# Kernel optimization log

Hardware: AMD Instinct MI355X
Metric: run time of the kernel (lower is better)

## Reference

```python
import jax, jax.numpy as jnp
import numpy as np

DIM = 2048
HIDDEN = 4096
BATCH = 4
SEQ = 2048


def setup_inputs() -> dict:
    key = jax.random.key(0)
    ks = jax.random.split(key, 4)
    scale_in = 1.0 / np.sqrt(DIM)
    scale_out = 1.0 / np.sqrt(HIDDEN)
    return {
        "x": jax.random.normal(ks[0], (BATCH, SEQ, DIM), dtype=jnp.float32),
        "W_in": jax.random.normal(ks[1], (HIDDEN, DIM), dtype=jnp.float32) * scale_in,
        "b_in": jnp.zeros((HIDDEN,), dtype=jnp.float32),
        "W_out": jax.random.normal(ks[2], (DIM, HIDDEN), dtype=jnp.float32) * scale_out,
        "b_out": jnp.zeros((DIM,), dtype=jnp.float32),
        "gamma": jnp.ones((HIDDEN,), dtype=jnp.float32),
        "beta": jnp.zeros((HIDDEN,), dtype=jnp.float32),
    }


def reference(x, W_in, b_in, W_out, b_out, gamma, beta):
    # Pre-project all timesteps in one GEMM: u[b,s,h] = input_proj(x[b,s,:])
    u = jnp.einsum("bsd,hd->bsh", x, W_in) + b_in  # [B,S,H]

    # Sequential elementwise recurrence: state = tanh(u_t + state*gamma + beta)
    def step(state, u_t):
        s = jnp.tanh(u_t + state * gamma + beta)
        return s, s

    init = jnp.zeros((x.shape[0], W_in.shape[0]), dtype=x.dtype)  # [B,H]
    _, states = jax.lax.scan(step, init, jnp.swapaxes(u, 0, 1))  # [S,B,H]
    states = jnp.swapaxes(states, 0, 1)  # [B,S,H]

    # Output projection in one GEMM (matches per-step out_proj then stack)
    y = jnp.einsum("bsh,dh->bsd", states, W_out) + b_out  # [B,S,D]
    return y
```

## Files before the change

### kernel.cpp

```cpp
#include <hip/hip_runtime.h>
#include <hip/hip_bf16.h>
#include <math.h>

#define B_ 4
#define S_ 2048
#define D_ 2048
#define H_ 4096
#define M_ (B_*S_)

#define SEG 128
#define WARM 48
#define P_ (S_/SEG)

typedef __bf16 bf16x8 __attribute__((ext_vector_type(8)));
typedef float f32x4 __attribute__((ext_vector_type(4)));

__device__ __forceinline__ float bf2f(unsigned short v) {
    union { unsigned u; float f; } x; x.u = ((unsigned)v) << 16; return x.f;
}
__device__ __forceinline__ unsigned short f2bf(float f) {
    union { float f; unsigned u; } x; x.f = f;
    unsigned u = x.u;
    unsigned r = (u + 0x7fffu + ((u >> 16) & 1u)) >> 16;
    return (unsigned short)r;
}

__device__ __forceinline__ float fast_exp2(float x) {
#if __has_builtin(__builtin_amdgcn_exp2f)
    return __builtin_amdgcn_exp2f(x);
#else
    return __builtin_exp2f(x);
#endif
}
__device__ __forceinline__ float fast_rcp(float x) {
    return __builtin_amdgcn_rcpf(x);
}

__global__ void cvt_f32_bf16(const float* __restrict__ in,
                             unsigned short* __restrict__ out, int n) {
    int i = (blockIdx.x * blockDim.x + threadIdx.x) * 8;
    if (i >= n) return;
    float4 a = *(const float4*)(in + i);
    float4 b = *(const float4*)(in + i + 4);
    ushort4 o0; o0.x = f2bf(a.x); o0.y = f2bf(a.y); o0.z = f2bf(a.z); o0.w = f2bf(a.w);
    ushort4 o1; o1.x = f2bf(b.x); o1.y = f2bf(b.y); o1.z = f2bf(b.z); o1.w = f2bf(b.w);
    *(ushort4*)(out + i) = o0;
    *(ushort4*)(out + i + 4) = o1;
}

__device__ __forceinline__ void async_cp16(const unsigned short* g, unsigned short* l) {
    __builtin_amdgcn_global_load_lds(
        (__attribute__((address_space(1))) void*)g,
        (__attribute__((address_space(3))) void*)l,
        16, 0, 0);
}

__device__ __forceinline__
void stage_tile(const unsigned short* Ag0, const unsigned short* Ag1,
                const unsigned short* Bg0, const unsigned short* Bg1,
                int kt, unsigned short* As, unsigned short* Bs,
                int c0, int c1) {
    async_cp16(Ag0 + kt, As + c0 * 8);
    async_cp16(Ag1 + kt, As + c1 * 8);
    async_cp16(Bg0 + kt, Bs + c0 * 8);
    async_cp16(Bg1 + kt, Bs + c1 * 8);
}

__device__ __forceinline__
void compute_tile(const unsigned short* As, const unsigned short* Bs,
                  int wr, int wc, int laneM, int laneK, f32x4 acc[4][4]) {
    bf16x8 af[4], bfr[4];
    #pragma unroll
    for (int i = 0; i < 4; ++i) {
        af[i]  = *(const bf16x8*)(As + (wr + i * 16 + laneM) * 32 + laneK);
        bfr[i] = *(const bf16x8*)(Bs + (wc + i * 16 + laneM) * 32 + laneK);
    }
    #pragma unroll
    for (int i = 0; i < 4; ++i)
        #pragma unroll
        for (int j = 0; j < 4; ++j)
            acc[i][j] = __builtin_amdgcn_mfma_f32_16x16x32_bf16(
                af[i], bfr[j], acc[i][j], 0, 0, 0);
}

template<bool OUT_BF16>
__device__ __forceinline__
void gemm_bt_body(const unsigned short* __restrict__ A,
                  const unsigned short* __restrict__ Bw,
                  const float* __restrict__ bias,
                  unsigned short* __restrict__ outB,
                  float* __restrict__ outF,
                  int M, int N, int K)
{
    __shared__ __align__(16) unsigned short As[2][128 * 32];
    __shared__ __align__(16) unsigned short Bs[2][128 * 32];

    const int tid  = threadIdx.x;
    const int lane = tid & 63;
    const int wave = tid >> 6;
    const int wr = (wave >> 1) * 64;
    const int wc = (wave & 1) * 64;

    const int row0 = blockIdx.y * 128;
    const int col0 = blockIdx.x * 128;

    const int c0 = tid, c1 = tid + 256;
    const int r0 = c0 >> 2, s0 = (c0 & 3) * 8;
    const int r1 = c1 >> 2, s1 = (c1 & 3) * 8;

    const unsigned short* Ag0 = A  + (size_t)(row0 + r0) * K + s0;
    const unsigned short* Ag1 = A  + (size_t)(row0 + r1) * K + s1;
    const unsigned short* Bg0 = Bw + (size_t)(col0 + r0) * K + s0;
    const unsigned short* Bg1 = Bw + (size_t)(col0 + r1) * K + s1;

    const int laneM = lane & 15;
    const int laneK = (lane >> 4) * 8;

    f32x4 acc[4][4];
    #pragma unroll
    for (int i = 0; i < 4; ++i)
        #pragma unroll
        for (int j = 0; j < 4; ++j)
            acc[i][j] = (f32x4){0.f, 0.f, 0.f, 0.f};

    stage_tile(Ag0, Ag1, Bg0, Bg1, 0, As[0], Bs[0], c0, c1);
    __syncthreads();

    for (int kt = 0; kt < K; kt += 64) {
        stage_tile(Ag0, Ag1, Bg0, Bg1, kt + 32, As[1], Bs[1], c0, c1);
        compute_tile(As[0], Bs[0], wr, wc, laneM, laneK, acc);
        __syncthreads();

        if (kt + 64 < K)
            stage_tile(Ag0, Ag1, Bg0, Bg1, kt + 64, As[0], Bs[0], c0, c1);
        compute_tile(As[1], Bs[1], wr, wc, laneM, laneK, acc);
        __syncthreads();
    }

    const int rQuad = (lane >> 4) * 4;
    #pragma unroll
    for (int j = 0; j < 4; ++j) {
        const int n = col0 + wc + j * 16 + laneM;
        const float bv = bias[n];
        #pragma unroll
        for (int i = 0; i < 4; ++i) {
            #pragma unroll
            for (int rr = 0; rr < 4; ++rr) {
                const int m = row0 + wr + i * 16 + rQuad + rr;
                const float v = acc[i][j][rr] + bv;
                if (OUT_BF16) outB[(size_t)m * N + n] = f2bf(v);
                else          outF[(size_t)m * N + n] = v;
            }
        }
    }
}

__global__ __launch_bounds__(256, 4)
void gemm_u(const unsigned short* __restrict__ A, const unsigned short* __restrict__ Bw,
            const float* __restrict__ bias, unsigned short* __restrict__ outB,
            int M, int N, int K) {
    gemm_bt_body<true>(A, Bw, bias, outB, nullptr, M, N, K);
}
__global__ __launch_bounds__(256, 4)
void gemm_y(const unsigned short* __restrict__ A, const unsigned short* __restrict__ Bw,
            const float* __restrict__ bias, float* __restrict__ outF,
            int M, int N, int K) {
    gemm_bt_body<false>(A, Bw, bias, nullptr, outF, M, N, K);
}

__global__ __launch_bounds__(256)
void recur_seg(const unsigned short* __restrict__ u,
               const float* __restrict__ gamma,
               const float* __restrict__ beta,
               unsigned short* __restrict__ st)
{
    const int tid = blockIdx.x * 256 + threadIdx.x;
    const int h   = tid & (H_ - 1);
    const int b   = (tid >> 12) & (B_ - 1);
    const int seg = tid >> 14;
    const int s0  = seg * SEG;
    const int sw  = (seg == 0) ? 0 : s0 - WARM;
    const int nst = s0 + SEG - sw;
    const float K2  = 2.885390082f;
    const float gk  = gamma[h] * K2;
    const float bek = beta[h]  * K2;
    float state = 0.f;

    size_t idx = ((size_t)b * S_ + sw) * H_ + h;
    float cur[16], nxt[16];
    #pragma unroll
    for (int k = 0; k < 16; ++k) cur[k] = bf2f(u[idx + (size_t)k * H_]);

    int s = sw;
    const int ngroups = nst >> 4;
    for (int g = 0; g < ngroups; ++g) {
        const size_t nidx = idx + (size_t)16 * H_;
        if (g + 1 < ngroups) {
            #pragma unroll
            for (int k = 0; k < 16; ++k) nxt[k] = bf2f(u[nidx + (size_t)k * H_]);
        }
        #pragma unroll
        for (int k = 0; k < 16; ++k) {
            const float c = fmaf(cur[k], K2, bek);
            const float t = fmaf(state, gk, c);
            const float e = fast_exp2(t);
            const float rr = fast_rcp(1.0f + e);
            state = fmaf(-2.0f, rr, 1.0f);
            if (s + k >= s0) st[idx + (size_t)k * H_] = f2bf(state);
        }
        idx = nidx; s += 16;
        #pragma unroll
        for (int k = 0; k < 16; ++k) cur[k] = nxt[k];
    }
}

extern "C" void kernel_launch(void* const* d_in, const int* in_sizes, int n_in,
                              void* d_out, int out_size, void* d_ws, size_t ws_size,
                              hipStream_t stream) {
    const float* x     = (const float*)d_in[0];
    const float* W_in  = (const float*)d_in[1];
    const float* b_in  = (const float*)d_in[2];
    const float* W_out = (const float*)d_in[3];
    const float* b_out = (const float*)d_in[4];
    const float* gamma = (const float*)d_in[5];
    const float* beta  = (const float*)d_in[6];
    float* y = (float*)d_out;

    unsigned short* x_b    = (unsigned short*)d_ws;
    unsigned short* win_b  = x_b    + (size_t)M_ * D_;
    unsigned short* wout_b = win_b  + (size_t)H_ * D_;
    unsigned short* u_b    = wout_b + (size_t)D_ * H_;
    unsigned short* st_b   = u_b    + (size_t)M_ * H_;

    cvt_f32_bf16<<<(M_ * D_) / 2048, 256, 0, stream>>>(x,     x_b,    M_ * D_);
    cvt_f32_bf16<<<(H_ * D_) / 2048, 256, 0, stream>>>(W_in,  win_b,  H_ * D_);
    cvt_f32_bf16<<<(D_ * H_) / 2048, 256, 0, stream>>>(W_out, wout_b, D_ * H_);

    dim3 g1(H_ / 128, M_ / 128);
    gemm_u<<<g1, 256, 0, stream>>>(x_b, win_b, b_in, u_b, M_, H_, D_);

    recur_seg<<<(P_ * B_ * H_) / 256, 256, 0, stream>>>(u_b, gamma, beta, st_b);

    dim3 g2(D_ / 128, M_ / 128);
    gemm_y<<<g2, 256, 0, stream>>>(st_b, wout_b, b_out, y, M_, D_, H_);
}
```

Before: 507.2 us.

## Rewrite GEMMs with 256x256 tiles, 8 waves, swizzled LDS and deeper async pipeline

Replaces the 128x128, 4-wave bf16 GEMM with a 256x256 block tile using 512 threads. Each wave computes a 128x64 sub-tile. Global-to-LDS async loads are split into half-tile stages issued several steps ahead with explicit vmcnt waits and raw barriers. An XOR swizzle on LDS offsets avoids bank conflicts, and s_setprio raises priority around the MFMA bursts. The aim is more data reuse per loaded byte and better overlap of loads with matrix math, at the cost of more registers, fewer blocks for the smaller output GEMM, and fragile hand-tuned wait counts.

```diff
diff --git a/kernel.cpp b/kernel.cpp
--- a/kernel.cpp
+++ b/kernel.cpp
@@ -55,98 +55,169 @@
         16, 0, 0);
 }
 
+__device__ __forceinline__ void fence_bar() {
+    asm volatile("" ::: "memory");
+    __builtin_amdgcn_s_barrier();
+    asm volatile("" ::: "memory");
+}
+
+template<int N>
+__device__ __forceinline__ void wait_vmcnt() {
+    if constexpr (N == 0)      asm volatile("s_waitcnt vmcnt(0)" ::: "memory");
+    else if constexpr (N == 4) asm volatile("s_waitcnt vmcnt(4)" ::: "memory");
+    else if constexpr (N == 6) asm volatile("s_waitcnt vmcnt(6)" ::: "memory");
+}
+
+
 __device__ __forceinline__
-void stage_tile(const unsigned short* Ag0, const unsigned short* Ag1,
-                const unsigned short* Bg0, const unsigned short* Bg1,
-                int kt, unsigned short* As, unsigned short* Bs,
-                int c0, int c1) {
-    async_cp16(Ag0 + kt, As + c0 * 8);
-    async_cp16(Ag1 + kt, As + c1 * 8);
-    async_cp16(Bg0 + kt, Bs + c0 * 8);
-    async_cp16(Bg1 + kt, Bs + c1 * 8);
+void stage_half(int g, int G, unsigned short (&lds)[2][2][2][8192],
+                const unsigned short* Asrc, const unsigned short* Bsrc,
+                int K, int sdst)
+{
+    if (g >= G) return;
+    const int tau = g >> 2;
+    const int mat = g & 1;
+    const int kh  = (g >> 1) & 1;
+    const unsigned short* src = (mat ? Bsrc : Asrc) + (size_t)tau * 64 + kh * 32;
+    unsigned short* dst = &lds[tau & 1][mat][kh][sdst];
+    async_cp16(src, dst);
+    async_cp16(src + (size_t)128 * K, dst + 4096);
 }
 
 __device__ __forceinline__
-void compute_tile(const unsigned short* As, const unsigned short* Bs,
-                  int wr, int wc, int laneM, int laneK, f32x4 acc[4][4]) {
-    bf16x8 af[4], bfr[4];
-    #pragma unroll
-    for (int i = 0; i < 4; ++i) {
-        af[i]  = *(const bf16x8*)(As + (wr + i * 16 + laneM) * 32 + laneK);
-        bfr[i] = *(const bf16x8*)(Bs + (wc + i * 16 + laneM) * 32 + laneK);
-    }
-    #pragma unroll
-    for (int i = 0; i < 4; ++i)
-        #pragma unroll
+void mfma16(const bf16x8* a, const bf16x8* b, f32x4 (*acc)[4]) {
+#pragma unroll
+    for (int i = 0; i < 4; ++i)
+#pragma unroll
         for (int j = 0; j < 4; ++j)
             acc[i][j] = __builtin_amdgcn_mfma_f32_16x16x32_bf16(
-                af[i], bfr[j], acc[i][j], 0, 0, 0);
+                a[i], b[j], acc[i][j], 0, 0, 0);
+}
+
+template<int BUF, int VP1, int VP3>
+__device__ __forceinline__
+void do_tile(int t, int G, unsigned short (&lds)[2][2][2][8192],
+             const unsigned short* Asrc, const unsigned short* Bsrc, int K,
+             int sdst, int aoff, int boff, f32x4 (*acc)[4])
+{
+    const int g0 = 4 * t + 5;
+    bf16x8 a[4], b[4];
+
+#pragma unroll
+    for (int j = 0; j < 4; ++j)
+        b[j] = *(const bf16x8*)(&lds[BUF][1][0][boff + j * 512]);
+#pragma unroll
+    for (int i = 0; i < 4; ++i)
+        a[i] = *(const bf16x8*)(&lds[BUF][0][0][aoff + i * 512]);
+    stage_half(g0 + 0, G, lds, Asrc, Bsrc, K, sdst);
+    fence_bar();
+    __builtin_amdgcn_s_setprio(1);
+    mfma16(a, b, acc);
+    __builtin_amdgcn_s_setprio(0);
+    fence_bar();
+
+#pragma unroll
+    for (int i = 0; i < 4; ++i)
+        a[i] = *(const bf16x8*)(&lds[BUF][0][0][aoff + (i + 4) * 512]);
+    stage_half(g0 + 1, G, lds, Asrc, Bsrc, K, sdst);
+    wait_vmcnt<VP1>();
+    fence_bar();
+    __builtin_amdgcn_s_setprio(1);
+    mfma16(a, b, acc + 4);
+    __builtin_amdgcn_s_setprio(0);
+    fence_bar();
+
+#pragma unroll
+    for (int j = 0; j < 4; ++j)
+        b[j] = *(const bf16x8*)(&lds[BUF][1][1][boff + j * 512]);
+#pragma unroll
+    for (int i = 0; i < 4; ++i)
+        a[i] = *(const bf16x8*)(&lds[BUF][0][1][aoff + i * 512]);
+    stage_half(g0 + 2, G, lds, Asrc, Bsrc, K, sdst);
+    fence_bar();
+    __builtin_amdgcn_s_setprio(1);
+    mfma16(a, b, acc);
+    __builtin_amdgcn_s_setprio(0);
+    fence_bar();
+
+#pragma unroll
+    for (int i = 0; i < 4; ++i)
+        a[i] = *(const bf16x8*)(&lds[BUF][0][1][aoff + (i + 4) * 512]);
+    stage_half(g0 + 3, G, lds, Asrc, Bsrc, K, sdst);
+    if constexpr (VP3 >= 0) wait_vmcnt<VP3>();
+    fence_bar();
+    __builtin_amdgcn_s_setprio(1);
+    mfma16(a, b, acc + 4);
+    __builtin_amdgcn_s_setprio(0);
+    fence_bar();
 }
 
 template<bool OUT_BF16>
 __device__ __forceinline__
-void gemm_bt_body(const unsigned short* __restrict__ A,
+void gemm256_body(const unsigned short* __restrict__ A,
                   const unsigned short* __restrict__ Bw,
                   const float* __restrict__ bias,
                   unsigned short* __restrict__ outB,
                   float* __restrict__ outF,
                   int M, int N, int K)
 {
-    __shared__ __align__(16) unsigned short As[2][128 * 32];
-    __shared__ __align__(16) unsigned short Bs[2][128 * 32];
+    __shared__ __align__(16) unsigned short lds[2][2][2][8192];
 
     const int tid  = threadIdx.x;
     const int lane = tid & 63;
     const int wave = tid >> 6;
-    const int wr = (wave >> 1) * 64;
-    const int wc = (wave & 1) * 64;
-
-    const int row0 = blockIdx.y * 128;
-    const int col0 = blockIdx.x * 128;
-
-    const int c0 = tid, c1 = tid + 256;
-    const int r0 = c0 >> 2, s0 = (c0 & 3) * 8;
-    const int r1 = c1 >> 2, s1 = (c1 & 3) * 8;
-
-    const unsigned short* Ag0 = A  + (size_t)(row0 + r0) * K + s0;
-    const unsigned short* Ag1 = A  + (size_t)(row0 + r1) * K + s1;
-    const unsigned short* Bg0 = Bw + (size_t)(col0 + r0) * K + s0;
-    const unsigned short* Bg1 = Bw + (size_t)(col0 + r1) * K + s1;
+    const int wm = wave >> 2;
+    const int wn = wave & 3;
+    const int row0 = blockIdx.y * 256;
+    const int col0 = blockIdx.x * 256;
+    const int NT = K >> 6;
+    const int G  = NT << 2;
+
+    const int srow = tid >> 2;
+    const int scol = ((tid & 3) ^ ((tid >> 3) & 3)) * 8;
+    const unsigned short* Asrc = A  + (size_t)(row0 + srow) * K + scol;
+    const unsigned short* Bsrc = Bw + (size_t)(col0 + srow) * K + scol;
+    const int sdst = tid * 8;
 
     const int laneM = lane & 15;
     const int laneK = (lane >> 4) * 8;
-
-    f32x4 acc[4][4];
-    #pragma unroll
-    for (int i = 0; i < 4; ++i)
-        #pragma unroll
+    const int swz   = ((laneM >> 1) & 3) << 3;
+    const int aoff  = (((wm * 128 + laneM) * 32 + laneK)) ^ swz;
+    const int boff  = (((wn * 64  + laneM) * 32 + laneK)) ^ swz;
+
+    f32x4 acc[8][4];
+#pragma unroll
+    for (int i = 0; i < 8; ++i)
+#pragma unroll
         for (int j = 0; j < 4; ++j)
             acc[i][j] = (f32x4){0.f, 0.f, 0.f, 0.f};
 
-    stage_tile(Ag0, Ag1, Bg0, Bg1, 0, As[0], Bs[0], c0, c1);
-    __syncthreads();
-
-    for (int kt = 0; kt < K; kt += 64) {
-        stage_tile(Ag0, Ag1, Bg0, Bg1, kt + 32, As[1], Bs[1], c0, c1);
-        compute_tile(As[0], Bs[0], wr, wc, laneM, laneK, acc);
-        __syncthreads();
-
-        if (kt + 64 < K)
-            stage_tile(Ag0, Ag1, Bg0, Bg1, kt + 64, As[0], Bs[0], c0, c1);
-        compute_tile(As[1], Bs[1], wr, wc, laneM, laneK, acc);
-        __syncthreads();
+    stage_half(0, G, lds, Asrc, Bsrc, K, sdst);
+    stage_half(1, G, lds, Asrc, Bsrc, K, sdst);
+    stage_half(2, G, lds, Asrc, Bsrc, K, sdst);
+    stage_half(3, G, lds, Asrc, Bsrc, K, sdst);
+    stage_half(4, G, lds, Asrc, Bsrc, K, sdst);
+    wait_vmcnt<6>();
+    fence_bar();
+
+    int t = 0;
+    for (; t < NT - 2; t += 2) {
+        do_tile<0, 6, 6>(t,     G, lds, Asrc, Bsrc, K, sdst, aoff, boff, acc);
+        do_tile<1, 6, 6>(t + 1, G, lds, Asrc, Bsrc, K, sdst, aoff, boff, acc);
     }
-
-    const int rQuad = (lane >> 4) * 4;
-    #pragma unroll
+    do_tile<0, 6, 4>(NT - 2, G, lds, Asrc, Bsrc, K, sdst, aoff, boff, acc);
+    do_tile<1, 0, -1>(NT - 1, G, lds, Asrc, Bsrc, K, sdst, aoff, boff, acc);
+
+    const int rQ = (lane >> 4) * 4;
+#pragma unroll
     for (int j = 0; j < 4; ++j) {
-        const int n = col0 + wc + j * 16 + laneM;
+        const int n = col0 + wn * 64 + j * 16 + laneM;
         const float bv = bias[n];
-        #pragma unroll
-        for (int i = 0; i < 4; ++i) {
-            #pragma unroll
+#pragma unroll
+        for (int i = 0; i < 8; ++i) {
+#pragma unroll
             for (int rr = 0; rr < 4; ++rr) {
-                const int m = row0 + wr + i * 16 + rQuad + rr;
+                const int m = row0 + wm * 128 + i * 16 + rQ + rr;
                 const float v = acc[i][j][rr] + bv;
                 if (OUT_BF16) outB[(size_t)m * N + n] = f2bf(v);
                 else          outF[(size_t)m * N + n] = v;
@@ -155,17 +226,17 @@
     }
 }
 
-__global__ __launch_bounds__(256, 4)
+__global__ __launch_bounds__(512, 2)
 void gemm_u(const unsigned short* __restrict__ A, const unsigned short* __restrict__ Bw,
             const float* __restrict__ bias, unsigned short* __restrict__ outB,
             int M, int N, int K) {
-    gemm_bt_body<true>(A, Bw, bias, outB, nullptr, M, N, K);
-}
-__global__ __launch_bounds__(256, 4)
+    gemm256_body<true>(A, Bw, bias, outB, nullptr, M, N, K);
+}
+__global__ __launch_bounds__(512, 2)
 void gemm_y(const unsigned short* __restrict__ A, const unsigned short* __restrict__ Bw,
             const float* __restrict__ bias, float* __restrict__ outF,
             int M, int N, int K) {
-    gemm_bt_body<false>(A, Bw, bias, nullptr, outF, M, N, K);
+    gemm256_body<false>(A, Bw, bias, nullptr, outF, M, N, K);
 }
 
 __global__ __launch_bounds__(256)
@@ -236,11 +307,11 @@
     cvt_f32_bf16<<<(H_ * D_) / 2048, 256, 0, stream>>>(W_in,  win_b,  H_ * D_);
     cvt_f32_bf16<<<(D_ * H_) / 2048, 256, 0, stream>>>(W_out, wout_b, D_ * H_);
 
-    dim3 g1(H_ / 128, M_ / 128);
-    gemm_u<<<g1, 256, 0, stream>>>(x_b, win_b, b_in, u_b, M_, H_, D_);
+    dim3 g1(H_ / 256, M_ / 256);
+    gemm_u<<<g1, 512, 0, stream>>>(x_b, win_b, b_in, u_b, M_, H_, D_);
 
     recur_seg<<<(P_ * B_ * H_) / 256, 256, 0, stream>>>(u_b, gamma, beta, st_b);
 
-    dim3 g2(D_ / 128, M_ / 128);
-    gemm_y<<<g2, 256, 0, stream>>>(st_b, wout_b, b_out, y, M_, D_, H_);
-}
+    dim3 g2(D_ / 256, M_ / 256);
+    gemm_y<<<g2, 512, 0, stream>>>(st_b, wout_b, b_out, y, M_, D_, H_);
+}
```

After: 486.2 us. 1.04x faster.
